# Performance work log

Hardware: AMD Instinct MI355X
Metric: run time of the kernel (lower is better)

## Reference

```python
import jax, jax.numpy as jnp
import numpy as np
import math

B, L = 4, 900
D_MODEL, D_STATE, D_INNER, DT_RANK = 256, 16, 512, 16


def setup_inputs() -> dict:
    key = jax.random.key(0)
    ks = jax.random.split(key, 10)
    nrm = lambda k, shape, s: jax.random.normal(k, shape, jnp.float32) * s
    hidden_states = jax.random.normal(ks[0], (B, L, D_MODEL), jnp.float32)
    W_in = nrm(ks[1], (2 * D_INNER, D_MODEL), D_MODEL ** -0.5)
    W_xproj = nrm(ks[2], (DT_RANK + 2 * D_STATE, D_INNER), D_INNER ** -0.5)
    s = DT_RANK ** -0.5
    W_dt = jax.random.uniform(ks[3], (D_INNER, DT_RANK), jnp.float32, -s, s)
    # dt bias init: inv_softplus of dt ~ LogUniform[1e-3, 0.1]
    dt = jnp.exp(jax.random.uniform(ks[4], (D_INNER,), jnp.float32)
                 * (math.log(0.1) - math.log(1e-3)) + math.log(1e-3))
    b_dt = dt + jnp.log(-jnp.expm1(-dt))
    A_log = jnp.broadcast_to(jnp.log(jnp.arange(1, D_STATE + 1, dtype=jnp.float32)),
                             (D_INNER, D_STATE))
    W_global = nrm(ks[5], (2 * D_INNER, 2 * D_INNER), (2 * D_INNER) ** -0.5)
    W_gate = nrm(ks[6], (2 * D_INNER, 2 * D_INNER), (2 * D_INNER) ** -0.5)
    W_out = nrm(ks[7], (D_MODEL, 2 * D_INNER), (2 * D_INNER) ** -0.5)
    return {
        'hidden_states': hidden_states, 'W_in': W_in, 'W_xproj': W_xproj,
        'W_dt': W_dt, 'b_dt': b_dt,
        'A_log_f': jnp.array(A_log), 'A_log_b': jnp.array(A_log),
        'D_f': jnp.ones(D_INNER, jnp.float32), 'D_b': jnp.ones(D_INNER, jnp.float32),
        'W_global': W_global, 'b_global': jnp.zeros(2 * D_INNER, jnp.float32),
        'W_gate': W_gate, 'b_gate': jnp.zeros(2 * D_INNER, jnp.float32),
        'W_out': W_out,
    }


def _selective_scan(u, delta, A, Bm, Cm, D):
    """u, delta: (b,l,d); Bm, Cm: (b,l,n); A: (d,n); D: (d,). Returns (b,l,d)."""
    dA = jnp.exp(jnp.einsum('bld,dn->lbdn', delta, A))          # discretized A
    dBu = jnp.einsum('bld,bln->lbdn', delta * u, Bm)             # dt*B*u
    Ct = jnp.transpose(Cm, (1, 0, 2))                            # (l,b,n)

    def step(h, inp):
        dA_t, dBu_t, c = inp
        h = dA_t * h + dBu_t                                     # (b,d,n)
        return h, jnp.einsum('bdn,bn->bd', h, c)

    h0 = jnp.zeros((u.shape[0], u.shape[2], A.shape[1]), u.dtype)
    _, ys = jax.lax.scan(step, h0, (dA, dBu, Ct))
    return jnp.transpose(ys, (1, 0, 2)) + D * u                  # D skip connection


def reference(hidden_states, W_in, W_xproj, W_dt, b_dt, A_log_f, A_log_b,
              D_f, D_b, W_global, b_global, W_gate, b_gate, W_out):
    silu = lambda t: t * jax.nn.sigmoid(t)
    xz = hidden_states @ W_in.T                                  # (b,l,2*di)
    x, z = jnp.split(xz, 2, axis=-1)
    x = silu(x)
    x_dbl = x @ W_xproj.T                                        # (b,l,r+2n)
    dt_r = x_dbl[..., :DT_RANK]
    Bm = x_dbl[..., DT_RANK:DT_RANK + D_STATE]
    Cm = x_dbl[..., DT_RANK + D_STATE:]
    dt = jax.nn.softplus(dt_r @ W_dt.T + b_dt)                   # (b,l,di)

    A_f = -jnp.exp(A_log_f)
    A_b = -jnp.exp(A_log_b)
    flip = lambda t: t[:, ::-1]
    y_f = _selective_scan(x, dt, A_f, Bm, Cm, D_f)
    y_b = flip(_selective_scan(flip(x), flip(dt), A_b, flip(Bm), flip(Cm), D_b))
    zg = silu(z)
    y = jnp.concatenate([y_f * zg, y_b * zg], axis=-1)           # (b,l,2*di)
    # global gate: pooled features -> global_proj -> y_gate_proj -> sigmoid
    g = jax.nn.sigmoid((y.mean(axis=1) @ W_global.T + b_global) @ W_gate.T + b_gate)
    y = y * g[:, None, :]
    return y @ W_out.T                                           # (b,l,d_model)
```

## Files before the change

### kernel.cpp

```cpp
#include <hip/hip_runtime.h>
#include <hip/hip_bf16.h>

#define BB 4
#define LL 900
#define DMODEL 256
#define DSTATE 16
#define DINNER 512
#define DTRANK 16
#define BL (BB*LL)
#define NC 75
#define LC 12

typedef __bf16 bf16x8 __attribute__((ext_vector_type(8)));
typedef __bf16 bf16x4 __attribute__((ext_vector_type(4)));
typedef float f32x4 __attribute__((ext_vector_type(4)));

__device__ __forceinline__ float silu_f(float v) { return v / (1.f + __expf(-v)); }

#define N_HID  (BL*DMODEL)
#define N_WIN  (2*DINNER*DMODEL)
#define N_WXP  (48*DINNER)
#define N_WOUT (DMODEL*2*DINNER)
#define N_WG   (2*DINNER*2*DINNER)
#define N_TOT  (N_HID+N_WIN+N_WXP+N_WOUT+2*N_WG)
__global__ void cvt_inputs(const float* __restrict__ hidden, const float* __restrict__ Win,
                           const float* __restrict__ Wxp, const float* __restrict__ Wout,
                           const float* __restrict__ Wglob, const float* __restrict__ Wgate,
                           __bf16* __restrict__ hh, __bf16* __restrict__ wih,
                           __bf16* __restrict__ wxh, __bf16* __restrict__ woh,
                           __bf16* __restrict__ wgb, __bf16* __restrict__ wtb)
{
    int idx = blockIdx.x * 256 + threadIdx.x;
    if (idx >= N_TOT) return;
    const float* src; __bf16* dst; int off;
    if (idx < N_HID)                              { src = hidden; dst = hh;  off = idx; }
    else if (idx < N_HID+N_WIN)                   { src = Win;    dst = wih; off = idx - N_HID; }
    else if (idx < N_HID+N_WIN+N_WXP)             { src = Wxp;    dst = wxh; off = idx - N_HID - N_WIN; }
    else if (idx < N_HID+N_WIN+N_WXP+N_WOUT)      { src = Wout;   dst = woh; off = idx - N_HID - N_WIN - N_WXP; }
    else if (idx < N_HID+N_WIN+N_WXP+N_WOUT+N_WG) { src = Wglob;  dst = wgb; off = idx - N_HID - N_WIN - N_WXP - N_WOUT; }
    else                                          { src = Wgate;  dst = wtb; off = idx - N_HID - N_WIN - N_WXP - N_WOUT - N_WG; }
    dst[off] = (__bf16)src[off];
}

__launch_bounds__(256)
__global__ void gemm_silu(const __bf16* __restrict__ A, const __bf16* __restrict__ B,
                          __bf16* __restrict__ xb, __bf16* __restrict__ zb)
{
    constexpr int WM = 3, WN = 2, K = 256, nk = K >> 5;
    constexpr int M = BL, N = 2 * DINNER;
    int wave = (blockIdx.x * 256 + threadIdx.x) >> 6;
    int ntN = N / (16 * WN);
    if (wave >= (M / (16 * WM)) * ntN) return;
    int tm = wave / ntN, tn = wave % ntN;
    int lane = threadIdx.x & 63, q = lane >> 4, r = lane & 15;

    const bf16x8* Ar[WM]; const bf16x8* Br[WN];
    #pragma unroll
    for (int mi = 0; mi < WM; ++mi)
        Ar[mi] = (const bf16x8*)(A + (size_t)(tm * 48 + mi * 16 + r) * K);
    #pragma unroll
    for (int ni = 0; ni < WN; ++ni)
        Br[ni] = (const bf16x8*)(B + (size_t)(tn * 32 + ni * 16 + r) * K);
    f32x4 acc[WM][WN];
    #pragma unroll
    for (int mi = 0; mi < WM; ++mi)
        #pragma unroll
        for (int ni = 0; ni < WN; ++ni) acc[mi][ni] = (f32x4){0.f,0.f,0.f,0.f};

    #pragma unroll
    for (int kk = 0; kk < nk; ++kk) {
        int idx = kk * 4 + q;
        bf16x8 av[WM], bv[WN];
        #pragma unroll
        for (int mi = 0; mi < WM; ++mi) av[mi] = Ar[mi][idx];
        #pragma unroll
        for (int ni = 0; ni < WN; ++ni) bv[ni] = Br[ni][idx];
        #pragma unroll
        for (int mi = 0; mi < WM; ++mi)
            #pragma unroll
            for (int ni = 0; ni < WN; ++ni)
                acc[mi][ni] = __builtin_amdgcn_mfma_f32_16x16x32_bf16(av[mi], bv[ni], acc[mi][ni], 0, 0, 0);
    }
    #pragma unroll
    for (int mi = 0; mi < WM; ++mi)
        #pragma unroll
        for (int ni = 0; ni < WN; ++ni) {
            int col = tn * 32 + ni * 16 + r;
            #pragma unroll
            for (int i = 0; i < 4; ++i) {
                int row = tm * 48 + mi * 16 + q * 4 + i;
                float s = silu_f(acc[mi][ni][i]);
                if (col < DINNER) xb[(size_t)row * DINNER + col] = (__bf16)s;
                else              zb[(size_t)row * DINNER + (col - DINNER)] = (__bf16)s;
            }
        }
}

__launch_bounds__(256)
__global__ void gemm2_dt(const __bf16* __restrict__ A, const __bf16* __restrict__ B,
                         const float* __restrict__ Wdt, const float* __restrict__ bdt,
                         float* __restrict__ dtBC, __bf16* __restrict__ dtb)
{
    constexpr int WN = 3, K = 512, KSL = 128, nk = KSL >> 5;
    __shared__ float lds[4][16 * 48];
    int tm = blockIdx.x;
    int wv = threadIdx.x >> 6, kOff = wv * KSL;
    int lane = threadIdx.x & 63, q = lane >> 4, r = lane & 15;

    const bf16x8* Ar = (const bf16x8*)(A + (size_t)(tm * 16 + r) * K + kOff);
    const bf16x8* Br[WN];
    #pragma unroll
    for (int ni = 0; ni < WN; ++ni)
        Br[ni] = (const bf16x8*)(B + (size_t)(ni * 16 + r) * K + kOff);
    f32x4 acc[WN];
    #pragma unroll
    for (int ni = 0; ni < WN; ++ni) acc[ni] = (f32x4){0.f,0.f,0.f,0.f};

    #pragma unroll
    for (int kk = 0; kk < nk; ++kk) {
        int idx = kk * 4 + q;
        bf16x8 av = Ar[idx];
        #pragma unroll
        for (int ni = 0; ni < WN; ++ni)
            acc[ni] = __builtin_amdgcn_mfma_f32_16x16x32_bf16(av, Br[ni][idx], acc[ni], 0, 0, 0);
    }
    #pragma unroll
    for (int ni = 0; ni < WN; ++ni) {
        int col = ni * 16 + r;
        #pragma unroll
        for (int i = 0; i < 4; ++i)
            lds[wv][(q * 4 + i) * 48 + col] = acc[ni][i];
    }
    __syncthreads();
    for (int e = threadIdx.x; e < 16 * 48; e += 256) {
        float s = lds[0][e] + lds[1][e] + lds[2][e] + lds[3][e];
        lds[0][e] = s;
        int row = e / 48, col = e % 48;
        dtBC[(size_t)(tm * 16 + row) * 48 + col] = s;
    }
    __syncthreads();
    for (int it = 0; it < 32; ++it) {
        int e = threadIdx.x + it * 256;
        int row = e >> 9, d = e & 511;
        const float* wr = Wdt + (size_t)d * DTRANK;
        float s = bdt[d];
        #pragma unroll
        for (int k = 0; k < DTRANK; ++k) s = fmaf(lds[0][row * 48 + k], wr[k], s);
        float dtv = (s > 15.f) ? s : __logf(1.f + __expf(s));
        dtb[(size_t)(tm * 16 + row) * DINNER + d] = (__bf16)dtv;
    }
}

__global__ void scan_pass1(const __bf16* __restrict__ dtb,
                           const __bf16* __restrict__ xb,
                           const float* __restrict__ dtBC,
                           const float* __restrict__ AlogF, const float* __restrict__ AlogB,
                           float* __restrict__ sdtBuf, __bf16* __restrict__ Qbuf)
{
    int b = blockIdx.z, dir = blockIdx.y;
    int c = blockIdx.x >> 2, dgrp = blockIdx.x & 3;
    int d = dgrp * 128 + threadIdx.x;
    const float* Alog = dir ? AlogB : AlogF;
    float a2[DSTATE];
    #pragma unroll
    for (int n = 0; n < DSTATE; ++n) a2[n] = -__expf(Alog[d * DSTATE + n]) * 1.44269504f;
    float h[DSTATE];
    #pragma unroll
    for (int n = 0; n < DSTATE; ++n) h[n] = 0.f;
    float sdt = 0.f;

    #pragma unroll 4
    for (int il = 0; il < LC; ++il) {
        int i = c * LC + il;
        int l = dir ? (LL - 1 - i) : i;
        size_t base = (size_t)b * LL + l;
        float dtv = (float)dtb[base * DINNER + d];
        float u = (float)xb[base * DINNER + d];
        float du = dtv * u;
        const f32x4* Bp = (const f32x4*)(dtBC + base * 48 + DTRANK);
        f32x4 Bq[4];
        #pragma unroll
        for (int j = 0; j < 4; ++j) Bq[j] = Bp[j];
        sdt += dtv;
        #pragma unroll
        for (int n = 0; n < DSTATE; ++n)
            h[n] = fmaf(exp2f(dtv * a2[n]), h[n], du * Bq[n >> 2][n & 3]);
    }
    int bd = b * 2 + dir;
    sdtBuf[((size_t)bd * NC + c) * DINNER + d] = sdt;
    size_t o = (((size_t)bd * NC + c) * DSTATE) * DINNER + d;
    #pragma unroll
    for (int n = 0; n < DSTATE; ++n)
        Qbuf[o + (size_t)n * DINNER] = (__bf16)h[n];
}

__global__ void scan_stitch(const float* __restrict__ sdtBuf,
                            const float* __restrict__ AlogF, const float* __restrict__ AlogB,
                            __bf16* __restrict__ Qbuf)
{
    int idx = blockIdx.x * 256 + threadIdx.x;
    int bd = idx >> 13;
    int rem = idx & 8191;
    int n = rem >> 9, d = rem & 511;
    const float* Alog = (bd & 1) ? AlogB : AlogF;
    float a2 = -__expf(Alog[d * DSTATE + n]) * 1.44269504f;
    size_t qbase = (size_t)bd * NC * 8192 + rem;
    size_t sbase = (size_t)bd * NC * DINNER + d;
    float H = 0.f;
    for (int cb = 0; cb < NC; cb += 15) {
        float Qv[15], Sv[15];
        #pragma unroll
        for (int j = 0; j < 15; ++j) {
            Qv[j] = (float)Qbuf[qbase + (size_t)(cb + j) * 8192];
            Sv[j] = sdtBuf[sbase + (size_t)(cb + j) * DINNER];
        }
        #pragma unroll
        for (int j = 0; j < 15; ++j) {
            Qbuf[qbase + (size_t)(cb + j) * 8192] = (__bf16)H;
            H = fmaf(exp2f(Sv[j] * a2), H, Qv[j]);
        }
    }
}

__global__ void scan_pass3(const __bf16* __restrict__ dtb,
                           const __bf16* __restrict__ xb,
                           const float* __restrict__ dtBC,
                           const float* __restrict__ AlogF, const float* __restrict__ AlogB,
                           const float* __restrict__ Df, const float* __restrict__ Db,
                           const __bf16* __restrict__ zb,
                           const __bf16* __restrict__ H0buf,
                           __bf16* __restrict__ yb,
                           float* __restrict__ partial)
{
    int b = blockIdx.z, dir = blockIdx.y;
    int c = blockIdx.x >> 2, dgrp = blockIdx.x & 3;
    int d = dgrp * 128 + threadIdx.x;
    const float* Alog = dir ? AlogB : AlogF;
    float a2[DSTATE];
    #pragma unroll
    for (int n = 0; n < DSTATE; ++n) a2[n] = -__expf(Alog[d * DSTATE + n]) * 1.44269504f;
    float Dd = dir ? Db[d] : Df[d];
    size_t o = (((size_t)(b * 2 + dir) * NC + c) * DSTATE) * DINNER + d;
    float h[DSTATE];
    #pragma unroll
    for (int n = 0; n < DSTATE; ++n) h[n] = (float)H0buf[o + (size_t)n * DINNER];
    float ysum = 0.f;

    #pragma unroll 4
    for (int il = 0; il < LC; ++il) {
        int i = c * LC + il;
        int l = dir ? (LL - 1 - i) : i;
        size_t base = (size_t)b * LL + l;
        float dtv = (float)dtb[base * DINNER + d];
        float u = (float)xb[base * DINNER + d];
        float du = dtv * u;
        const f32x4* Bp = (const f32x4*)(dtBC + base * 48 + DTRANK);
        f32x4 Bq[4], Cq[4];
        #pragma unroll
        for (int j = 0; j < 4; ++j) Bq[j] = Bp[j];
        #pragma unroll
        for (int j = 0; j < 4; ++j) Cq[j] = Bp[4 + j];
        float p = 0.f;
        #pragma unroll
        for (int n = 0; n < DSTATE; ++n) {
            h[n] = fmaf(exp2f(dtv * a2[n]), h[n], du * Bq[n >> 2][n & 3]);
            p = fmaf(h[n], Cq[n >> 2][n & 3], p);
        }
        float zg = (float)zb[base * DINNER + d];
        float yv = (p + Dd * u) * zg;
        size_t yo = base * (2 * DINNER) + dir * DINNER + d;
        yb[yo] = (__bf16)yv;
        ysum += yv;
    }
    partial[((size_t)b * NC + c) * 1024 + dir * DINNER + d] = ysum;
}

__global__ void mean2(const float* __restrict__ partial, float* __restrict__ ymean)
{
    int i = blockIdx.x * 256 + threadIdx.x;
    int b = i >> 10, ch = i & 1023;
    float s = 0.f;
    #pragma unroll 5
    for (int c = 0; c < NC; ++c) s += partial[((size_t)b * NC + c) * 1024 + ch];
    ymean[i] = s / (float)LL;
}

template<int SIG>
__global__ void gemv1024(const float* __restrict__ vin,
                         const __bf16* __restrict__ W,
                         const float* __restrict__ bias,
                         float* __restrict__ vout)
{
    int wv = (blockIdx.x * blockDim.x + threadIdx.x) >> 6;
    int b = wv >> 10, j = wv & 1023;
    int lane = threadIdx.x & 63;
    const __bf16* wr = W + (size_t)j * 1024;
    const float* vr = vin + (size_t)b * 1024;
    float s = 0.f;
    for (int k = lane; k < 1024; k += 64) s = fmaf(vr[k], (float)wr[k], s);
    #pragma unroll
    for (int o = 32; o; o >>= 1) s += __shfl_xor(s, o);
    if (lane == 0) {
        s += bias[j];
        vout[wv] = SIG ? (1.f / (1.f + __expf(-s))) : s;
    }
}

__global__ void scale_y(__bf16* __restrict__ yb, const float* __restrict__ g)
{
    int idx = blockIdx.x * 256 + threadIdx.x;
    int e = idx * 8;
    int ch = e & 1023;
    int b = (e >> 10) / LL;
    bf16x8 v = reinterpret_cast<bf16x8*>(yb)[idx];
    const f32x4* gp = (const f32x4*)(g + b * 1024 + ch);
    f32x4 g0 = gp[0], g1 = gp[1];
    #pragma unroll
    for (int j = 0; j < 4; ++j) v[j] = (__bf16)((float)v[j] * g0[j]);
    #pragma unroll
    for (int j = 0; j < 4; ++j) v[4 + j] = (__bf16)((float)v[4 + j] * g1[j]);
    reinterpret_cast<bf16x8*>(yb)[idx] = v;
}

__launch_bounds__(256)
__global__ void gemm8_comb(const __bf16* __restrict__ A, const __bf16* __restrict__ B,
                           float* __restrict__ out)
{
    constexpr int WM = 3, WN = 2, K = 1024, KSL = 512, nk = KSL >> 5;
    constexpr int N = DMODEL, ntN = N / (16 * WN);
    __shared__ float lds[2][2][48 * 32];
    int wv = threadIdx.x >> 6;
    int tLoc = wv >> 1, ks = wv & 1;
    int tIdx = blockIdx.x * 2 + tLoc;
    int tm = tIdx / ntN, tn = tIdx % ntN;
    int kOff = ks * KSL;
    int lane = threadIdx.x & 63, q = lane >> 4, r = lane & 15;

    const bf16x8* Ar[WM]; const bf16x8* Br[WN];
    #pragma unroll
    for (int mi = 0; mi < WM; ++mi)
        Ar[mi] = (const bf16x8*)(A + (size_t)(tm * 48 + mi * 16 + r) * K + kOff);
    #pragma unroll
    for (int ni = 0; ni < WN; ++ni)
        Br[ni] = (const bf16x8*)(B + (size_t)(tn * 32 + ni * 16 + r) * K + kOff);
    f32x4 acc[WM][WN];
    #pragma unroll
    for (int mi = 0; mi < WM; ++mi)
        #pragma unroll
        for (int ni = 0; ni < WN; ++ni) acc[mi][ni] = (f32x4){0.f,0.f,0.f,0.f};

    #pragma unroll
    for (int kk = 0; kk < nk; ++kk) {
        int idx = kk * 4 + q;
        bf16x8 av[WM], bv[WN];
        #pragma unroll
        for (int mi = 0; mi < WM; ++mi) av[mi] = Ar[mi][idx];
        #pragma unroll
        for (int ni = 0; ni < WN; ++ni) bv[ni] = Br[ni][idx];
        #pragma unroll
        for (int mi = 0; mi < WM; ++mi)
            #pragma unroll
            for (int ni = 0; ni < WN; ++ni)
                acc[mi][ni] = __builtin_amdgcn_mfma_f32_16x16x32_bf16(av[mi], bv[ni], acc[mi][ni], 0, 0, 0);
    }
    #pragma unroll
    for (int mi = 0; mi < WM; ++mi)
        #pragma unroll
        for (int ni = 0; ni < WN; ++ni) {
            int col = ni * 16 + r;
            #pragma unroll
            for (int i = 0; i < 4; ++i)
                lds[tLoc][ks][(mi * 16 + q * 4 + i) * 32 + col] = acc[mi][ni][i];
        }
    __syncthreads();
    for (int e = threadIdx.x; e < 2 * 1536; e += 256) {
        int tl = (e >= 1536) ? 1 : 0;
        int idx = e - tl * 1536;
        int row = idx >> 5, col = idx & 31;
        int tg = blockIdx.x * 2 + tl;
        int gm = (tg / ntN) * 48 + row, gn = (tg % ntN) * 32 + col;
        out[(size_t)gm * N + gn] = lds[tl][0][idx] + lds[tl][1][idx];
    }
}

extern "C" void kernel_launch(void* const* d_in, const int* in_sizes, int n_in,
                              void* d_out, int out_size, void* d_ws, size_t ws_size,
                              hipStream_t stream)
{
    const float* hidden  = (const float*)d_in[0];
    const float* W_in    = (const float*)d_in[1];
    const float* W_xproj = (const float*)d_in[2];
    const float* W_dt    = (const float*)d_in[3];
    const float* b_dt    = (const float*)d_in[4];
    const float* A_log_f = (const float*)d_in[5];
    const float* A_log_b = (const float*)d_in[6];
    const float* D_f     = (const float*)d_in[7];
    const float* D_b     = (const float*)d_in[8];
    const float* W_glob  = (const float*)d_in[9];
    const float* b_glob  = (const float*)d_in[10];
    const float* W_gate  = (const float*)d_in[11];
    const float* b_gate  = (const float*)d_in[12];
    const float* W_out   = (const float*)d_in[13];
    float* out = (float*)d_out;

    char* w = (char*)d_ws;
    __bf16* xb    = (__bf16*)w; w += (size_t)BL * DINNER * 2;
    __bf16* zb    = (__bf16*)w; w += (size_t)BL * DINNER * 2;
    float* dtBC   = (float*)w;  w += (size_t)BL * 48 * 4;
    __bf16* dtb   = (__bf16*)w; w += (size_t)BL * DINNER * 2;
    __bf16* yb    = (__bf16*)w; w += (size_t)BL * 2 * DINNER * 2;
    float* partial= (float*)w;  w += (size_t)BB * NC * 1024 * 4;
    float* ymean  = (float*)w;  w += (size_t)BB * 1024 * 4;
    float* t1     = (float*)w;  w += (size_t)BB * 1024 * 4;
    float* gbuf   = (float*)w;  w += (size_t)BB * 1024 * 4;
    __bf16* hh    = (__bf16*)w; w += (size_t)N_HID * 2;
    __bf16* wih   = (__bf16*)w; w += (size_t)N_WIN * 2;
    __bf16* wxh   = (__bf16*)w; w += (size_t)N_WXP * 2;
    __bf16* woh   = (__bf16*)w; w += (size_t)N_WOUT * 2;
    __bf16* wgb   = (__bf16*)w; w += (size_t)N_WG * 2;
    __bf16* wtb   = (__bf16*)w; w += (size_t)N_WG * 2;
    float* sdtBuf = (float*)w;  w += (size_t)BB * 2 * NC * DINNER * 4;
    __bf16* Qbuf  = (__bf16*)w; w += (size_t)BB * 2 * NC * DSTATE * DINNER * 2;

    cvt_inputs<<<dim3((N_TOT + 255) / 256), dim3(256), 0, stream>>>(
        hidden, W_in, W_xproj, W_out, W_glob, W_gate, hh, wih, wxh, woh, wgb, wtb);
    gemm_silu<<<dim3(600), dim3(256), 0, stream>>>(hh, wih, xb, zb);
    gemm2_dt<<<dim3(225), dim3(256), 0, stream>>>(xb, wxh, W_dt, b_dt, dtBC, dtb);
    scan_pass1<<<dim3(NC * 4, 2, BB), dim3(128), 0, stream>>>(
        dtb, xb, dtBC, A_log_f, A_log_b, sdtBuf, Qbuf);
    scan_stitch<<<dim3(256), dim3(256), 0, stream>>>(sdtBuf, A_log_f, A_log_b, Qbuf);
    scan_pass3<<<dim3(NC * 4, 2, BB), dim3(128), 0, stream>>>(
        dtb, xb, dtBC, A_log_f, A_log_b, D_f, D_b, zb, Qbuf, yb, partial);
    mean2<<<dim3(16), dim3(256), 0, stream>>>(partial, ymean);
    gemv1024<0><<<dim3(1024), dim3(256), 0, stream>>>(ymean, wgb, b_glob, t1);
    gemv1024<1><<<dim3(1024), dim3(256), 0, stream>>>(t1, wtb, b_gate, gbuf);
    scale_y<<<dim3(BL * 1024 / 8 / 256), dim3(256), 0, stream>>>(yb, gbuf);
    gemm8_comb<<<dim3(300), dim3(256), 0, stream>>>(yb, woh, out);
}
```

Measured before the change: 219.7 us.

## Fuse gate scaling into output GEMM and use atomic mean accumulation

```diff
diff --git a/kernel.cpp b/kernel.cpp
--- a/kernel.cpp
+++ b/kernel.cpp
@@ -21,24 +21,21 @@
 #define N_WIN  (2*DINNER*DMODEL)
 #define N_WXP  (48*DINNER)
 #define N_WOUT (DMODEL*2*DINNER)
-#define N_WG   (2*DINNER*2*DINNER)
-#define N_TOT  (N_HID+N_WIN+N_WXP+N_WOUT+2*N_WG)
+#define N_TOT  (N_HID+N_WIN+N_WXP+N_WOUT)
 __global__ void cvt_inputs(const float* __restrict__ hidden, const float* __restrict__ Win,
                            const float* __restrict__ Wxp, const float* __restrict__ Wout,
-                           const float* __restrict__ Wglob, const float* __restrict__ Wgate,
                            __bf16* __restrict__ hh, __bf16* __restrict__ wih,
                            __bf16* __restrict__ wxh, __bf16* __restrict__ woh,
-                           __bf16* __restrict__ wgb, __bf16* __restrict__ wtb)
+                           float* __restrict__ ymean)
 {
     int idx = blockIdx.x * 256 + threadIdx.x;
+    if (idx < BB * 1024) ymean[idx] = 0.f;
     if (idx >= N_TOT) return;
     const float* src; __bf16* dst; int off;
-    if (idx < N_HID)                              { src = hidden; dst = hh;  off = idx; }
-    else if (idx < N_HID+N_WIN)                   { src = Win;    dst = wih; off = idx - N_HID; }
-    else if (idx < N_HID+N_WIN+N_WXP)             { src = Wxp;    dst = wxh; off = idx - N_HID - N_WIN; }
-    else if (idx < N_HID+N_WIN+N_WXP+N_WOUT)      { src = Wout;   dst = woh; off = idx - N_HID - N_WIN - N_WXP; }
-    else if (idx < N_HID+N_WIN+N_WXP+N_WOUT+N_WG) { src = Wglob;  dst = wgb; off = idx - N_HID - N_WIN - N_WXP - N_WOUT; }
-    else                                          { src = Wgate;  dst = wtb; off = idx - N_HID - N_WIN - N_WXP - N_WOUT - N_WG; }
+    if (idx < N_HID)                        { src = hidden; dst = hh;  off = idx; }
+    else if (idx < N_HID+N_WIN)             { src = Win;    dst = wih; off = idx - N_HID; }
+    else if (idx < N_HID+N_WIN+N_WXP)       { src = Wxp;    dst = wxh; off = idx - N_HID - N_WIN; }
+    else                                    { src = Wout;   dst = woh; off = idx - N_HID - N_WIN - N_WXP; }
     dst[off] = (__bf16)src[off];
 }
 
@@ -230,7 +227,7 @@
                            const __bf16* __restrict__ zb,
                            const __bf16* __restrict__ H0buf,
                            __bf16* __restrict__ yb,
-                           float* __restrict__ partial)
+                           float* __restrict__ ymean)
 {
     int b = blockIdx.z, dir = blockIdx.y;
     int c = blockIdx.x >> 2, dgrp = blockIdx.x & 3;
@@ -272,74 +269,52 @@
         yb[yo] = (__bf16)yv;
         ysum += yv;
     }
-    partial[((size_t)b * NC + c) * 1024 + dir * DINNER + d] = ysum;
-}
-
-__global__ void mean2(const float* __restrict__ partial, float* __restrict__ ymean)
-{
-    int i = blockIdx.x * 256 + threadIdx.x;
-    int b = i >> 10, ch = i & 1023;
-    float s = 0.f;
-    #pragma unroll 5
-    for (int c = 0; c < NC; ++c) s += partial[((size_t)b * NC + c) * 1024 + ch];
-    ymean[i] = s / (float)LL;
+    atomicAdd(&ymean[b * 1024 + dir * DINNER + d], ysum);
 }
 
 template<int SIG>
 __global__ void gemv1024(const float* __restrict__ vin,
-                         const __bf16* __restrict__ W,
+                         const float* __restrict__ W,
                          const float* __restrict__ bias,
-                         float* __restrict__ vout)
+                         float* __restrict__ vout, float scl)
 {
     int wv = (blockIdx.x * blockDim.x + threadIdx.x) >> 6;
     int b = wv >> 10, j = wv & 1023;
     int lane = threadIdx.x & 63;
-    const __bf16* wr = W + (size_t)j * 1024;
+    const float* wr = W + (size_t)j * 1024;
     const float* vr = vin + (size_t)b * 1024;
     float s = 0.f;
-    for (int k = lane; k < 1024; k += 64) s = fmaf(vr[k], (float)wr[k], s);
+    for (int k = lane; k < 1024; k += 64) s = fmaf(vr[k], wr[k], s);
     #pragma unroll
     for (int o = 32; o; o >>= 1) s += __shfl_xor(s, o);
     if (lane == 0) {
-        s += bias[j];
+        s = s * scl + bias[j];
         vout[wv] = SIG ? (1.f / (1.f + __expf(-s))) : s;
     }
-}
-
-__global__ void scale_y(__bf16* __restrict__ yb, const float* __restrict__ g)
-{
-    int idx = blockIdx.x * 256 + threadIdx.x;
-    int e = idx * 8;
-    int ch = e & 1023;
-    int b = (e >> 10) / LL;
-    bf16x8 v = reinterpret_cast<bf16x8*>(yb)[idx];
-    const f32x4* gp = (const f32x4*)(g + b * 1024 + ch);
-    f32x4 g0 = gp[0], g1 = gp[1];
-    #pragma unroll
-    for (int j = 0; j < 4; ++j) v[j] = (__bf16)((float)v[j] * g0[j]);
-    #pragma unroll
-    for (int j = 0; j < 4; ++j) v[4 + j] = (__bf16)((float)v[4 + j] * g1[j]);
-    reinterpret_cast<bf16x8*>(yb)[idx] = v;
 }
 
 __launch_bounds__(256)
 __global__ void gemm8_comb(const __bf16* __restrict__ A, const __bf16* __restrict__ B,
+                           const float* __restrict__ g,
                            float* __restrict__ out)
 {
-    constexpr int WM = 3, WN = 2, K = 1024, KSL = 512, nk = KSL >> 5;
+    constexpr int WM = 3, WN = 2, K = 1024, KSL = 256, nk = KSL >> 5;
     constexpr int N = DMODEL, ntN = N / (16 * WN);
-    __shared__ float lds[2][2][48 * 32];
-    int wv = threadIdx.x >> 6;
-    int tLoc = wv >> 1, ks = wv & 1;
-    int tIdx = blockIdx.x * 2 + tLoc;
+    __shared__ float lds[4][48 * 32];
+    int ks = threadIdx.x >> 6;
+    int tIdx = blockIdx.x;
     int tm = tIdx / ntN, tn = tIdx % ntN;
     int kOff = ks * KSL;
     int lane = threadIdx.x & 63, q = lane >> 4, r = lane & 15;
 
     const bf16x8* Ar[WM]; const bf16x8* Br[WN];
-    #pragma unroll
-    for (int mi = 0; mi < WM; ++mi)
-        Ar[mi] = (const bf16x8*)(A + (size_t)(tm * 48 + mi * 16 + r) * K + kOff);
+    const float* gp[WM];
+    #pragma unroll
+    for (int mi = 0; mi < WM; ++mi) {
+        int grow = tm * 48 + mi * 16 + r;
+        Ar[mi] = (const bf16x8*)(A + (size_t)grow * K + kOff);
+        gp[mi] = g + (grow / LL) * 1024 + kOff;
+    }
     #pragma unroll
     for (int ni = 0; ni < WN; ++ni)
         Br[ni] = (const bf16x8*)(B + (size_t)(tn * 32 + ni * 16 + r) * K + kOff);
@@ -354,7 +329,16 @@
         int idx = kk * 4 + q;
         bf16x8 av[WM], bv[WN];
         #pragma unroll
-        for (int mi = 0; mi < WM; ++mi) av[mi] = Ar[mi][idx];
+        for (int mi = 0; mi < WM; ++mi) {
+            bf16x8 a = Ar[mi][idx];
+            const f32x4* gv = (const f32x4*)(gp[mi] + idx * 8);
+            f32x4 g0 = gv[0], g1 = gv[1];
+            #pragma unroll
+            for (int j = 0; j < 4; ++j) a[j] = (__bf16)((float)a[j] * g0[j]);
+            #pragma unroll
+            for (int j = 0; j < 4; ++j) a[4 + j] = (__bf16)((float)a[4 + j] * g1[j]);
+            av[mi] = a;
+        }
         #pragma unroll
         for (int ni = 0; ni < WN; ++ni) bv[ni] = Br[ni][idx];
         #pragma unroll
@@ -370,16 +354,13 @@
             int col = ni * 16 + r;
             #pragma unroll
             for (int i = 0; i < 4; ++i)
-                lds[tLoc][ks][(mi * 16 + q * 4 + i) * 32 + col] = acc[mi][ni][i];
+                lds[ks][(mi * 16 + q * 4 + i) * 32 + col] = acc[mi][ni][i];
         }
     __syncthreads();
-    for (int e = threadIdx.x; e < 2 * 1536; e += 256) {
-        int tl = (e >= 1536) ? 1 : 0;
-        int idx = e - tl * 1536;
-        int row = idx >> 5, col = idx & 31;
-        int tg = blockIdx.x * 2 + tl;
-        int gm = (tg / ntN) * 48 + row, gn = (tg % ntN) * 32 + col;
-        out[(size_t)gm * N + gn] = lds[tl][0][idx] + lds[tl][1][idx];
+    for (int e = threadIdx.x; e < 1536; e += 256) {
+        int row = e >> 5, col = e & 31;
+        int gm = tm * 48 + row, gn = tn * 32 + col;
+        out[(size_t)gm * N + gn] = lds[0][e] + lds[1][e] + lds[2][e] + lds[3][e];
     }
 }
 
@@ -409,7 +390,6 @@
     float* dtBC   = (float*)w;  w += (size_t)BL * 48 * 4;
     __bf16* dtb   = (__bf16*)w; w += (size_t)BL * DINNER * 2;
     __bf16* yb    = (__bf16*)w; w += (size_t)BL * 2 * DINNER * 2;
-    float* partial= (float*)w;  w += (size_t)BB * NC * 1024 * 4;
     float* ymean  = (float*)w;  w += (size_t)BB * 1024 * 4;
     float* t1     = (float*)w;  w += (size_t)BB * 1024 * 4;
     float* gbuf   = (float*)w;  w += (size_t)BB * 1024 * 4;
@@ -417,23 +397,19 @@
     __bf16* wih   = (__bf16*)w; w += (size_t)N_WIN * 2;
     __bf16* wxh   = (__bf16*)w; w += (size_t)N_WXP * 2;
     __bf16* woh   = (__bf16*)w; w += (size_t)N_WOUT * 2;
-    __bf16* wgb   = (__bf16*)w; w += (size_t)N_WG * 2;
-    __bf16* wtb   = (__bf16*)w; w += (size_t)N_WG * 2;
     float* sdtBuf = (float*)w;  w += (size_t)BB * 2 * NC * DINNER * 4;
     __bf16* Qbuf  = (__bf16*)w; w += (size_t)BB * 2 * NC * DSTATE * DINNER * 2;
 
     cvt_inputs<<<dim3((N_TOT + 255) / 256), dim3(256), 0, stream>>>(
-        hidden, W_in, W_xproj, W_out, W_glob, W_gate, hh, wih, wxh, woh, wgb, wtb);
+        hidden, W_in, W_xproj, W_out, hh, wih, wxh, woh, ymean);
     gemm_silu<<<dim3(600), dim3(256), 0, stream>>>(hh, wih, xb, zb);
     gemm2_dt<<<dim3(225), dim3(256), 0, stream>>>(xb, wxh, W_dt, b_dt, dtBC, dtb);
     scan_pass1<<<dim3(NC * 4, 2, BB), dim3(128), 0, stream>>>(
         dtb, xb, dtBC, A_log_f, A_log_b, sdtBuf, Qbuf);
     scan_stitch<<<dim3(256), dim3(256), 0, stream>>>(sdtBuf, A_log_f, A_log_b, Qbuf);
     scan_pass3<<<dim3(NC * 4, 2, BB), dim3(128), 0, stream>>>(
-        dtb, xb, dtBC, A_log_f, A_log_b, D_f, D_b, zb, Qbuf, yb, partial);
-    mean2<<<dim3(16), dim3(256), 0, stream>>>(partial, ymean);
-    gemv1024<0><<<dim3(1024), dim3(256), 0, stream>>>(ymean, wgb, b_glob, t1);
-    gemv1024<1><<<dim3(1024), dim3(256), 0, stream>>>(t1, wtb, b_gate, gbuf);
-    scale_y<<<dim3(BL * 1024 / 8 / 256), dim3(256), 0, stream>>>(yb, gbuf);
-    gemm8_comb<<<dim3(300), dim3(256), 0, stream>>>(yb, woh, out);
-}
+        dtb, xb, dtBC, A_log_f, A_log_b, D_f, D_b, zb, Qbuf, yb, ymean);
+    gemv1024<0><<<dim3(1024), dim3(256), 0, stream>>>(ymean, W_glob, b_glob, t1, 1.f / (float)LL);
+    gemv1024<1><<<dim3(1024), dim3(256), 0, stream>>>(t1, W_gate, b_gate, gbuf, 1.f);
+    gemm8_comb<<<dim3(600), dim3(256), 0, stream>>>(yb, woh, gbuf, out);
+}
```

Measured after the change: 208.2 us. -5.2%, faster.
